# Performance work log

Hardware: AMD Instinct MI355X
Metric: run time of the kernel (lower is better)

## Reference

```python
import jax, jax.numpy as jnp
import numpy as np

MARGIN = 0.25
SCALE = 64.0
OP = 1.0 + MARGIN
ON = -MARGIN
DELTA_P = 1.0 - MARGIN
DELTA_N = MARGIN
NEG_FILL = -1e4  # effectively -inf for these logits (|logit| < ~300)

B, D = 8192, 1024
N_IDS = 512


def setup_inputs() -> dict:
    key = jax.random.key(0)
    k1, k2 = jax.random.split(key)
    inputs = jax.random.normal(k1, (B, D), dtype=jnp.float32)
    targets = jax.random.randint(k2, (B,), 0, N_IDS, dtype=jnp.int64)
    return {"inputs": inputs, "targets": targets}


def reference(inputs, targets):
    # L2-normalize embeddings (torch F.normalize uses eps=1e-12 clamp on norm)
    norm = jnp.maximum(jnp.linalg.norm(inputs, axis=1, keepdims=True), 1e-12)
    x = inputs / norm
    sim = x @ x.T  # [B, B] cosine similarities

    same = targets[:, None] == targets[None, :]
    eye = jnp.eye(targets.shape[0], dtype=bool)
    pos_mask = same & ~eye
    neg_mask = ~same

    sim_sg = jax.lax.stop_gradient(sim)  # .detach() in original
    ap = jnp.maximum(OP - sim_sg, 0.0)
    an = jnp.maximum(sim_sg - ON, 0.0)

    logit_p = -ap * (sim - DELTA_P) * SCALE
    logit_n = an * (sim - DELTA_N) * SCALE

    lse_p = jax.nn.logsumexp(jnp.where(pos_mask, logit_p, NEG_FILL), axis=1)
    lse_n = jax.nn.logsumexp(jnp.where(neg_mask, logit_n, NEG_FILL), axis=1)

    loss_i = jax.nn.softplus(lse_n + lse_p)  # [B]
    valid = pos_mask.any(axis=1) & neg_mask.any(axis=1)

    total = jnp.sum(jnp.where(valid, loss_i, 0.0))
    count = jnp.maximum(jnp.sum(valid), 1)
    return total / count
```

## Files before the change

### kernel.cpp

```cpp
#include <hip/hip_runtime.h>
#include <hip/hip_bf16.h>
#include <math.h>

#define THREADS 256
typedef unsigned short ushortT;
typedef __attribute__((ext_vector_type(8))) short bf16x8;
typedef __attribute__((ext_vector_type(4))) float f32x4;

__device__ __forceinline__ void async16(const ushortT* g, ushortT* l) {
  __builtin_amdgcn_global_load_lds(
      (const __attribute__((address_space(1))) unsigned int*)g,
      (__attribute__((address_space(3))) unsigned int*)l, 16, 0, 0);
}

__device__ __forceinline__ ushortT f2bf(float f) {
  __hip_bfloat16 h = __float2bfloat16(f);
  return *reinterpret_cast<ushortT*>(&h);
}

__global__ __launch_bounds__(THREADS) void k_prep(const float* __restrict__ x,
                                                  ushortT* __restrict__ xn, int D) {
  __shared__ float red[4];
  const int row = blockIdx.x;
  const int tid = threadIdx.x;
  const int gid = row * (D / 4) + tid;
  const float4 v = reinterpret_cast<const float4*>(x)[gid];
  float s = v.x * v.x + v.y * v.y + v.z * v.z + v.w * v.w;
  #pragma unroll
  for (int off = 32; off; off >>= 1) s += __shfl_xor(s, off);
  if ((tid & 63) == 0) red[tid >> 6] = s;
  __syncthreads();
  const float tot = red[0] + red[1] + red[2] + red[3];
  const float rn = 1.0f / fmaxf(sqrtf(tot), 1e-12f);
  ushort4 o;
  o.x = f2bf(v.x * rn); o.y = f2bf(v.y * rn);
  o.z = f2bf(v.z * rn); o.w = f2bf(v.w * rn);
  reinterpret_cast<ushort4*>(xn)[gid] = o;
}

__global__ __launch_bounds__(THREADS, 4) void k_main_mfma(const ushortT* __restrict__ xn,
                                                          const int* __restrict__ tgt,
                                                          float4* __restrict__ partial,
                                                          int D, int nb) {
  __shared__ ushortT Asm[2][128 * 32];
  __shared__ ushortT Bsm[2][128 * 32];

  const int tid = threadIdx.x;
  const int lane = tid & 63;
  const int w = tid >> 6;

  const int b = blockIdx.x;
  int bi = (int)((2.f * nb + 1.f -
                  sqrtf((2.f * nb + 1.f) * (2.f * nb + 1.f) - 8.f * (float)b)) * 0.5f);
  while ((bi + 1) * (2 * nb - bi) / 2 <= b) ++bi;
  while (bi * (2 * nb - bi + 1) / 2 > b) --bi;
  const int bj = bi + (b - bi * (2 * nb - bi + 1) / 2);
  const bool isdiag = (bi == bj);

  const int i0 = bi * 128, j0 = bj * 128;
  const int wr = (w >> 1) * 64, wc = (w & 1) * 64;

  const int sr = lane & 15, sc = lane >> 4;
  const ushortT* gA0 = xn + (size_t)(i0 + w * 16 + sr) * D + sc * 8;
  const ushortT* gA1 = gA0 + (size_t)64 * D;
  const ushortT* gB0 = xn + (size_t)(j0 + w * 16 + sr) * D + sc * 8;
  const ushortT* gB1 = gB0 + (size_t)64 * D;
  const int lo0 = w * 512;
  const int lo1 = (w + 4) * 512;

  const int aoff = ((w >> 1) * 4) * 512 + lane * 8;
  const int boff = ((w & 1) * 4) * 512 + lane * 8;

  f32x4 acc[4][4];
  #pragma unroll
  for (int mt = 0; mt < 4; ++mt)
    #pragma unroll
    for (int nt = 0; nt < 4; ++nt)
      acc[mt][nt] = (f32x4){0.f, 0.f, 0.f, 0.f};

  async16(gA0, &Asm[0][lo0]);
  async16(gA1, &Asm[0][lo1]);
  if (!isdiag) {
    async16(gB0, &Bsm[0][lo0]);
    async16(gB1, &Bsm[0][lo1]);
  }
  __syncthreads();

  const int kiters = D / 32;
  for (int kk = 0; kk < kiters; ++kk) {
    const int cur = kk & 1;
    if (kk + 1 < kiters) {
      const size_t ko = (size_t)(kk + 1) * 32;
      async16(gA0 + ko, &Asm[cur ^ 1][lo0]);
      async16(gA1 + ko, &Asm[cur ^ 1][lo1]);
      if (!isdiag) {
        async16(gB0 + ko, &Bsm[cur ^ 1][lo0]);
        async16(gB1 + ko, &Bsm[cur ^ 1][lo1]);
      }
    }
    const ushortT* Ab = &Asm[cur][0];
    const ushortT* Bb = isdiag ? &Asm[cur][0] : &Bsm[cur][0];
    bf16x8 afr[4], bfr[4];
    #pragma unroll
    for (int mt = 0; mt < 4; ++mt)
      afr[mt] = *reinterpret_cast<const bf16x8*>(&Ab[aoff + mt * 512]);
    #pragma unroll
    for (int nt = 0; nt < 4; ++nt)
      bfr[nt] = *reinterpret_cast<const bf16x8*>(&Bb[boff + nt * 512]);
    #pragma unroll
    for (int mt = 0; mt < 4; ++mt)
      #pragma unroll
      for (int nt = 0; nt < 4; ++nt)
        acc[mt][nt] = __builtin_amdgcn_mfma_f32_16x16x32_bf16(afr[mt], bfr[nt], acc[mt][nt], 0, 0, 0);
    __syncthreads();
  }

  const int q = lane >> 4, c = lane & 15;
  int tj[4];
  #pragma unroll
  for (int nt = 0; nt < 4; ++nt) tj[nt] = tgt[j0 + wc + nt * 16 + c];
  int tir[16];
  #pragma unroll
  for (int mt = 0; mt < 4; ++mt) {
    const int4 t4 = *reinterpret_cast<const int4*>(tgt + i0 + wr + mt * 16 + q * 4);
    tir[mt * 4 + 0] = t4.x; tir[mt * 4 + 1] = t4.y;
    tir[mt * 4 + 2] = t4.z; tir[mt * 4 + 3] = t4.w;
  }

  #pragma unroll
  for (int mt = 0; mt < 4; ++mt) {
    #pragma unroll
    for (int reg = 0; reg < 4; ++reg) {
      const int i = i0 + wr + mt * 16 + q * 4 + reg;
      const int ti = tir[mt * 4 + reg];
      float m = -1e30f, sn = 0.f;
      float sel[4];
      #pragma unroll
      for (int nt = 0; nt < 4; ++nt) {
        const float s = acc[mt][nt][reg];
        const int j = j0 + wc + nt * 16 + c;
        const bool same = (tj[nt] == ti);
        const bool vpos = same && (j != i);
        const float lp = (fminf(s, 1.25f) - 1.25f) * fmaf(s, 64.f, -48.f);
        const float sv = vpos ? lp : -2e30f;
        sel[nt] = sv;
        m = fmaxf(m, sv);
        const float ln = (fmaxf(s, -0.25f) + 0.25f) * fmaf(s, 64.f, -16.f);
        const float en = __expf(ln);
        sn += same ? 0.f : en;
      }
      #pragma unroll
      for (int off = 1; off < 16; off <<= 1) m = fmaxf(m, __shfl_xor(m, off));
      float sp = 0.f;
      #pragma unroll
      for (int nt = 0; nt < 4; ++nt) sp += __expf(sel[nt] - m);
      #pragma unroll
      for (int off = 1; off < 16; off <<= 1) {
        sp += __shfl_xor(sp, off);
        sn += __shfl_xor(sn, off);
      }
      if (c == 0) {
        float4 o; o.x = m; o.y = sp; o.z = 0.f; o.w = sn;
        partial[((size_t)i * nb + bj) * 2 + (w & 1)] = o;
      }
    }
  }

  if (!isdiag) {
    #pragma unroll
    for (int nt = 0; nt < 4; ++nt) {
      const int jt = tj[nt];
      const int jrow = j0 + wc + nt * 16 + c;
      float m = -1e30f, sn = 0.f;
      float sel[16];
      #pragma unroll
      for (int mt = 0; mt < 4; ++mt) {
        #pragma unroll
        for (int reg = 0; reg < 4; ++reg) {
          const float s = acc[mt][nt][reg];
          const bool same = (tir[mt * 4 + reg] == jt);
          const float lp = (fminf(s, 1.25f) - 1.25f) * fmaf(s, 64.f, -48.f);
          const float sv = same ? lp : -2e30f;
          sel[mt * 4 + reg] = sv;
          m = fmaxf(m, sv);
          const float ln = (fmaxf(s, -0.25f) + 0.25f) * fmaf(s, 64.f, -16.f);
          const float en = __expf(ln);
          sn += same ? 0.f : en;
        }
      }
      m = fmaxf(m, __shfl_xor(m, 16));
      m = fmaxf(m, __shfl_xor(m, 32));
      float sp = 0.f;
      #pragma unroll
      for (int k = 0; k < 16; ++k) sp += __expf(sel[k] - m);
      sp += __shfl_xor(sp, 16); sp += __shfl_xor(sp, 32);
      sn += __shfl_xor(sn, 16); sn += __shfl_xor(sn, 32);
      if (lane < 16) {
        float4 o; o.x = m; o.y = sp; o.z = 0.f; o.w = sn;
        partial[((size_t)jrow * nb + bi) * 2 + (w >> 1)] = o;
      }
    }
  }
}

__global__ __launch_bounds__(THREADS) void k_reduce(const float4* __restrict__ partial,
                                                    float* __restrict__ row_loss) {
  const int lane = threadIdx.x & 63;
  const int row = blockIdx.x * 4 + (threadIdx.x >> 6);
  const float4 a = partial[(size_t)row * 128 + lane];
  const float4 b = partial[(size_t)row * 128 + 64 + lane];
  float mp = fmaxf(a.x, b.x);
  float sp = a.y * __expf(a.x - mp) + b.y * __expf(b.x - mp);
  float sn = a.w + b.w;
  #pragma unroll
  for (int off = 1; off < 64; off <<= 1) {
    const float m2 = __shfl_xor(mp, off), s2 = __shfl_xor(sp, off);
    const float nm = fmaxf(mp, m2);
    sp = sp * __expf(mp - nm) + s2 * __expf(m2 - nm);
    mp = nm;
    sn += __shfl_xor(sn, off);
  }
  if (lane == 0) {
    float loss = -1.0f;
    if (sp > 0.f && sn > 0.f) {
      const float z = mp + logf(sp) + logf(sn);
      loss = (z > 0.f) ? (z + log1pf(__expf(-z))) : log1pf(__expf(z));
    }
    row_loss[row] = loss;
  }
}

__global__ __launch_bounds__(THREADS) void k_final(const float* __restrict__ row_loss,
                                                   float* __restrict__ out, int B) {
  __shared__ float ssum[4];
  __shared__ float scnt[4];
  const int tid = threadIdx.x;
  float sum = 0.f, cnt = 0.f;
  for (int i = tid; i < B; i += THREADS) {
    const float l = row_loss[i];
    if (l >= 0.f) { sum += l; cnt += 1.f; }
  }
  #pragma unroll
  for (int off = 32; off; off >>= 1) {
    sum += __shfl_xor(sum, off);
    cnt += __shfl_xor(cnt, off);
  }
  if ((tid & 63) == 0) { ssum[tid >> 6] = sum; scnt[tid >> 6] = cnt; }
  __syncthreads();
  if (tid == 0) {
    float ts = 0.f, tc = 0.f;
    #pragma unroll
    for (int w = 0; w < 4; ++w) { ts += ssum[w]; tc += scnt[w]; }
    out[0] = ts / fmaxf(tc, 1.f);
  }
}

extern "C" void kernel_launch(void* const* d_in, const int* in_sizes, int n_in,
                              void* d_out, int out_size, void* d_ws, size_t ws_size,
                              hipStream_t stream) {
  const float* x = (const float*)d_in[0];
  const int* tgt = (const int*)d_in[1];
  float* out = (float*)d_out;
  const int B = in_sizes[1];
  const int D = in_sizes[0] / B;
  const int nb = B / 128;

  ushortT* xn = (ushortT*)d_ws;
  float4* partial = (float4*)((char*)d_ws + (size_t)B * D * 2);
  float* row_loss = (float*)((char*)d_ws + (size_t)B * D * 2 + (size_t)B * 2 * nb * 16);

  k_prep<<<B, THREADS, 0, stream>>>(x, xn, D);
  k_main_mfma<<<nb * (nb + 1) / 2, THREADS, 0, stream>>>(xn, tgt, partial, D, nb);
  k_reduce<<<B / 4, THREADS, 0, stream>>>(partial, row_loss);
  k_final<<<1, THREADS, 0, stream>>>(row_loss, out, B);
}
```

Before: 259.6 us.

## Swizzle triangular tile order and merge half-tile partials in LDS before store

Replaces the closed-form triangular block mapping with a super-tile (8x8 groups) ordering so that concurrently running blocks share row/column strips in cache. The two per-wave-column partial (max, sum) records are combined in shared memory, reusing the A tile buffer, and one float4 per row per tile is written in a column-major [nb][B] layout. This halves the partial-buffer writes and lets the reduce kernel read one record per lane. The cost is an extra __syncthreads, more index arithmetic per block, and a mapping that hardcodes nb=64 (36 super-tiles of 8).

```diff
diff --git a/kernel.cpp b/kernel.cpp
--- a/kernel.cpp
+++ b/kernel.cpp
@@ -41,7 +41,7 @@
 __global__ __launch_bounds__(THREADS, 4) void k_main_mfma(const ushortT* __restrict__ xn,
                                                           const int* __restrict__ tgt,
                                                           float4* __restrict__ partial,
-                                                          int D, int nb) {
+                                                          int D, int B) {
   __shared__ ushortT Asm[2][128 * 32];
   __shared__ ushortT Bsm[2][128 * 32];
 
@@ -50,11 +50,28 @@
   const int w = tid >> 6;
 
   const int b = blockIdx.x;
-  int bi = (int)((2.f * nb + 1.f -
-                  sqrtf((2.f * nb + 1.f) * (2.f * nb + 1.f) - 8.f * (float)b)) * 0.5f);
-  while ((bi + 1) * (2 * nb - bi) / 2 <= b) ++bi;
-  while (bi * (2 * nb - bi + 1) / 2 > b) --bi;
-  const int bj = bi + (b - bi * (2 * nb - bi + 1) / 2);
+  int base = 0, SI = 0, SJ = 0, found = 0;
+  for (int x = 0; x < 8 && !found; ++x) {
+    for (int ss = x; ss < 36; ss += 8) {
+      int si = 0, rem = ss;
+      while (rem >= 8 - si) { rem -= 8 - si; ++si; }
+      const int sj = si + rem;
+      const int size = (si == sj) ? 36 : 64;
+      if (b < base + size) { SI = si; SJ = sj; found = 1; break; }
+      base += size;
+    }
+  }
+  const int l = b - base;
+  int li, lj;
+  if (SI == SJ) {
+    int t = l, row = 0;
+    while (t >= 8 - row) { t -= 8 - row; ++row; }
+    li = row; lj = row + t;
+  } else {
+    li = l >> 3; lj = l & 7;
+  }
+  const int bi = SI * 8 + li;
+  const int bj = SJ * 8 + lj;
   const bool isdiag = (bi == bj);
 
   const int i0 = bi * 128, j0 = bj * 128;
@@ -127,11 +144,15 @@
     tir[mt * 4 + 2] = t4.z; tir[mt * 4 + 3] = t4.w;
   }
 
+  float4* eo1 = reinterpret_cast<float4*>(&Asm[0][0]);
+  float4* eo2 = reinterpret_cast<float4*>(&Asm[0][2048]);
+
   #pragma unroll
   for (int mt = 0; mt < 4; ++mt) {
     #pragma unroll
     for (int reg = 0; reg < 4; ++reg) {
-      const int i = i0 + wr + mt * 16 + q * 4 + reg;
+      const int il = wr + mt * 16 + q * 4 + reg;
+      const int i = i0 + il;
       const int ti = tir[mt * 4 + reg];
       float m = -1e30f, sn = 0.f;
       float sel[4];
@@ -160,8 +181,8 @@
         sn += __shfl_xor(sn, off);
       }
       if (c == 0) {
-        float4 o; o.x = m; o.y = sp; o.z = 0.f; o.w = sn;
-        partial[((size_t)i * nb + bj) * 2 + (w & 1)] = o;
+        float4 o; o.x = m; o.y = sp; o.z = sn; o.w = 0.f;
+        eo1[il * 2 + (w & 1)] = o;
       }
     }
   }
@@ -170,7 +191,6 @@
     #pragma unroll
     for (int nt = 0; nt < 4; ++nt) {
       const int jt = tj[nt];
-      const int jrow = j0 + wc + nt * 16 + c;
       float m = -1e30f, sn = 0.f;
       float sel[16];
       #pragma unroll
@@ -196,22 +216,43 @@
       sp += __shfl_xor(sp, 16); sp += __shfl_xor(sp, 32);
       sn += __shfl_xor(sn, 16); sn += __shfl_xor(sn, 32);
       if (lane < 16) {
-        float4 o; o.x = m; o.y = sp; o.z = 0.f; o.w = sn;
-        partial[((size_t)jrow * nb + bi) * 2 + (w >> 1)] = o;
-      }
-    }
+        float4 o; o.x = m; o.y = sp; o.z = sn; o.w = 0.f;
+        eo2[(wc + nt * 16 + lane) * 2 + (w >> 1)] = o;
+      }
+    }
+  }
+
+  __syncthreads();
+
+  if (tid < 128) {
+    const float4 a = eo1[tid * 2], bb = eo1[tid * 2 + 1];
+    const float m = fmaxf(a.x, bb.x);
+    float4 o;
+    o.x = m;
+    o.y = a.y * __expf(a.x - m) + bb.y * __expf(bb.x - m);
+    o.z = a.z + bb.z;
+    o.w = 0.f;
+    partial[(size_t)bj * B + i0 + tid] = o;
+  } else if (!isdiag) {
+    const int t = tid - 128;
+    const float4 a = eo2[t * 2], bb = eo2[t * 2 + 1];
+    const float m = fmaxf(a.x, bb.x);
+    float4 o;
+    o.x = m;
+    o.y = a.y * __expf(a.x - m) + bb.y * __expf(bb.x - m);
+    o.z = a.z + bb.z;
+    o.w = 0.f;
+    partial[(size_t)bi * B + j0 + t] = o;
   }
 }
 
 __global__ __launch_bounds__(THREADS) void k_reduce(const float4* __restrict__ partial,
-                                                    float* __restrict__ row_loss) {
+                                                    float* __restrict__ row_loss,
+                                                    int B) {
   const int lane = threadIdx.x & 63;
   const int row = blockIdx.x * 4 + (threadIdx.x >> 6);
-  const float4 a = partial[(size_t)row * 128 + lane];
-  const float4 b = partial[(size_t)row * 128 + 64 + lane];
-  float mp = fmaxf(a.x, b.x);
-  float sp = a.y * __expf(a.x - mp) + b.y * __expf(b.x - mp);
-  float sn = a.w + b.w;
+  const float4 p = partial[(size_t)lane * B + row];
+  float mp = p.x, sp = p.y, sn = p.z;
   #pragma unroll
   for (int off = 1; off < 64; off <<= 1) {
     const float m2 = __shfl_xor(mp, off), s2 = __shfl_xor(sp, off);
@@ -267,10 +308,10 @@
 
   ushortT* xn = (ushortT*)d_ws;
   float4* partial = (float4*)((char*)d_ws + (size_t)B * D * 2);
-  float* row_loss = (float*)((char*)d_ws + (size_t)B * D * 2 + (size_t)B * 2 * nb * 16);
+  float* row_loss = (float*)((char*)d_ws + (size_t)B * D * 2 + (size_t)nb * B * 16);
 
   k_prep<<<B, THREADS, 0, stream>>>(x, xn, D);
-  k_main_mfma<<<nb * (nb + 1) / 2, THREADS, 0, stream>>>(xn, tgt, partial, D, nb);
-  k_reduce<<<B / 4, THREADS, 0, stream>>>(partial, row_loss);
+  k_main_mfma<<<nb * (nb + 1) / 2, THREADS, 0, stream>>>(xn, tgt, partial, D, B);
+  k_reduce<<<B / 4, THREADS, 0, stream>>>(partial, row_loss, B);
   k_final<<<1, THREADS, 0, stream>>>(row_loss, out, B);
 }
```

Measured after the change: 261.9 us. No clear change (+0.9%).

## Use 256x128 tiles with per-wave 64x128 MFMA subtiles and transposed partials

Applied to the files above, without the earlier changes.

Each block now computes a 256-row by 128-column tile of the upper-triangular similarity matrix. Each wave owns 64 rows across all 128 columns, so B fragments are shared across more MFMAs and each block issues fewer loads per output. Column-side partials are combined across waves in shared memory before being written, and the partial buffer is laid out column-block-major so k_reduce reads one entry per lane. The per-row logits are recomputed in a second pass instead of being held in a sel array. The cost is a larger accumulator, 128 floats per thread, with occupancy lowered to 2 waves per SIMD. Diagonal-straddling tiles also recompute some redundant lower-triangle work.

```diff
diff --git a/kernel.cpp b/kernel.cpp
--- a/kernel.cpp
+++ b/kernel.cpp
@@ -38,91 +38,98 @@
   reinterpret_cast<ushort4*>(xn)[gid] = o;
 }
 
-__global__ __launch_bounds__(THREADS, 4) void k_main_mfma(const ushortT* __restrict__ xn,
+__global__ __launch_bounds__(THREADS, 2) void k_main_mfma(const ushortT* __restrict__ xn,
                                                           const int* __restrict__ tgt,
                                                           float4* __restrict__ partial,
-                                                          int D, int nb) {
-  __shared__ ushortT Asm[2][128 * 32];
-  __shared__ ushortT Bsm[2][128 * 32];
+                                                          int D, int B) {
+  __shared__ ushortT Asm[2][16 * 512];
+  __shared__ ushortT Bsm[2][8 * 512];
 
   const int tid = threadIdx.x;
   const int lane = tid & 63;
   const int w = tid >> 6;
 
+  const int NRB = B / 256;
+  const int C1 = 2 * NRB + 1;
   const int b = blockIdx.x;
-  int bi = (int)((2.f * nb + 1.f -
-                  sqrtf((2.f * nb + 1.f) * (2.f * nb + 1.f) - 8.f * (float)b)) * 0.5f);
-  while ((bi + 1) * (2 * nb - bi) / 2 <= b) ++bi;
-  while (bi * (2 * nb - bi + 1) / 2 > b) --bi;
-  const int bj = bi + (b - bi * (2 * nb - bi + 1) / 2);
-  const bool isdiag = (bi == bj);
-
-  const int i0 = bi * 128, j0 = bj * 128;
-  const int wr = (w >> 1) * 64, wc = (w & 1) * 64;
+  int rb = (int)((C1 - sqrtf((float)(C1 * C1 - 4 * b))) * 0.5f);
+  while (rb * (C1 - rb) > b) --rb;
+  while ((rb + 1) * (C1 - rb - 1) <= b) ++rb;
+  const int cb = 2 * rb + (b - rb * (C1 - rb));
+  const bool ndiag = (cb <= 2 * rb + 1);
+
+  const int i0 = rb * 256, j0 = cb * 128;
 
   const int sr = lane & 15, sc = lane >> 4;
-  const ushortT* gA0 = xn + (size_t)(i0 + w * 16 + sr) * D + sc * 8;
-  const ushortT* gA1 = gA0 + (size_t)64 * D;
-  const ushortT* gB0 = xn + (size_t)(j0 + w * 16 + sr) * D + sc * 8;
-  const ushortT* gB1 = gB0 + (size_t)64 * D;
-  const int lo0 = w * 512;
-  const int lo1 = (w + 4) * 512;
-
-  const int aoff = ((w >> 1) * 4) * 512 + lane * 8;
-  const int boff = ((w & 1) * 4) * 512 + lane * 8;
-
-  f32x4 acc[4][4];
+  const ushortT* gA[4];
+  #pragma unroll
+  for (int t = 0; t < 4; ++t)
+    gA[t] = xn + (size_t)(i0 + 16 * (4 * w + t) + sr) * D + sc * 8;
+  const ushortT* gB[2];
+  #pragma unroll
+  for (int u = 0; u < 2; ++u)
+    gB[u] = xn + (size_t)(j0 + 16 * (w + 4 * u) + sr) * D + sc * 8;
+
+  f32x4 acc[4][8];
   #pragma unroll
   for (int mt = 0; mt < 4; ++mt)
     #pragma unroll
-    for (int nt = 0; nt < 4; ++nt)
+    for (int nt = 0; nt < 8; ++nt)
       acc[mt][nt] = (f32x4){0.f, 0.f, 0.f, 0.f};
 
-  async16(gA0, &Asm[0][lo0]);
-  async16(gA1, &Asm[0][lo1]);
-  if (!isdiag) {
-    async16(gB0, &Bsm[0][lo0]);
-    async16(gB1, &Bsm[0][lo1]);
+  #pragma unroll
+  for (int t = 0; t < 4; ++t) async16(gA[t], &Asm[0][(4 * w + t) * 512]);
+  if (!ndiag) {
+    #pragma unroll
+    for (int u = 0; u < 2; ++u) async16(gB[u], &Bsm[0][(w + 4 * u) * 512]);
   }
   __syncthreads();
 
+  const int boffg = ndiag ? (cb - 2 * rb) * 8 : 0;
   const int kiters = D / 32;
   for (int kk = 0; kk < kiters; ++kk) {
     const int cur = kk & 1;
     if (kk + 1 < kiters) {
       const size_t ko = (size_t)(kk + 1) * 32;
-      async16(gA0 + ko, &Asm[cur ^ 1][lo0]);
-      async16(gA1 + ko, &Asm[cur ^ 1][lo1]);
-      if (!isdiag) {
-        async16(gB0 + ko, &Bsm[cur ^ 1][lo0]);
-        async16(gB1 + ko, &Bsm[cur ^ 1][lo1]);
+      #pragma unroll
+      for (int t = 0; t < 4; ++t)
+        async16(gA[t] + ko, &Asm[cur ^ 1][(4 * w + t) * 512]);
+      if (!ndiag) {
+        #pragma unroll
+        for (int u = 0; u < 2; ++u)
+          async16(gB[u] + ko, &Bsm[cur ^ 1][(w + 4 * u) * 512]);
       }
     }
     const ushortT* Ab = &Asm[cur][0];
-    const ushortT* Bb = isdiag ? &Asm[cur][0] : &Bsm[cur][0];
-    bf16x8 afr[4], bfr[4];
+    const ushortT* Bb = ndiag ? &Asm[cur][boffg * 512] : &Bsm[cur][0];
+    bf16x8 afr[4];
     #pragma unroll
     for (int mt = 0; mt < 4; ++mt)
-      afr[mt] = *reinterpret_cast<const bf16x8*>(&Ab[aoff + mt * 512]);
-    #pragma unroll
-    for (int nt = 0; nt < 4; ++nt)
-      bfr[nt] = *reinterpret_cast<const bf16x8*>(&Bb[boff + nt * 512]);
-    #pragma unroll
-    for (int mt = 0; mt < 4; ++mt)
-      #pragma unroll
-      for (int nt = 0; nt < 4; ++nt)
-        acc[mt][nt] = __builtin_amdgcn_mfma_f32_16x16x32_bf16(afr[mt], bfr[nt], acc[mt][nt], 0, 0, 0);
+      afr[mt] = *reinterpret_cast<const bf16x8*>(&Ab[(4 * w + mt) * 512 + lane * 8]);
+    #pragma unroll
+    for (int h = 0; h < 2; ++h) {
+      bf16x8 bfr[4];
+      #pragma unroll
+      for (int n4 = 0; n4 < 4; ++n4)
+        bfr[n4] = *reinterpret_cast<const bf16x8*>(&Bb[(h * 4 + n4) * 512 + lane * 8]);
+      #pragma unroll
+      for (int mt = 0; mt < 4; ++mt)
+        #pragma unroll
+        for (int n4 = 0; n4 < 4; ++n4)
+          acc[mt][h * 4 + n4] =
+              __builtin_amdgcn_mfma_f32_16x16x32_bf16(afr[mt], bfr[n4], acc[mt][h * 4 + n4], 0, 0, 0);
+    }
     __syncthreads();
   }
 
   const int q = lane >> 4, c = lane & 15;
-  int tj[4];
-  #pragma unroll
-  for (int nt = 0; nt < 4; ++nt) tj[nt] = tgt[j0 + wc + nt * 16 + c];
+  int tj[8];
+  #pragma unroll
+  for (int nt = 0; nt < 8; ++nt) tj[nt] = tgt[j0 + nt * 16 + c];
   int tir[16];
   #pragma unroll
   for (int mt = 0; mt < 4; ++mt) {
-    const int4 t4 = *reinterpret_cast<const int4*>(tgt + i0 + wr + mt * 16 + q * 4);
+    const int4 t4 = *reinterpret_cast<const int4*>(tgt + i0 + w * 64 + mt * 16 + q * 4);
     tir[mt * 4 + 0] = t4.x; tir[mt * 4 + 1] = t4.y;
     tir[mt * 4 + 2] = t4.z; tir[mt * 4 + 3] = t4.w;
   }
@@ -131,87 +138,105 @@
   for (int mt = 0; mt < 4; ++mt) {
     #pragma unroll
     for (int reg = 0; reg < 4; ++reg) {
-      const int i = i0 + wr + mt * 16 + q * 4 + reg;
+      const int i = i0 + w * 64 + mt * 16 + q * 4 + reg;
       const int ti = tir[mt * 4 + reg];
       float m = -1e30f, sn = 0.f;
-      float sel[4];
-      #pragma unroll
-      for (int nt = 0; nt < 4; ++nt) {
+      #pragma unroll
+      for (int nt = 0; nt < 8; ++nt) {
         const float s = acc[mt][nt][reg];
-        const int j = j0 + wc + nt * 16 + c;
+        const int j = j0 + nt * 16 + c;
         const bool same = (tj[nt] == ti);
-        const bool vpos = same && (j != i);
+        const bool v = same && (j != i);
         const float lp = (fminf(s, 1.25f) - 1.25f) * fmaf(s, 64.f, -48.f);
-        const float sv = vpos ? lp : -2e30f;
-        sel[nt] = sv;
-        m = fmaxf(m, sv);
+        m = v ? fmaxf(m, lp) : m;
         const float ln = (fmaxf(s, -0.25f) + 0.25f) * fmaf(s, 64.f, -16.f);
-        const float en = __expf(ln);
-        sn += same ? 0.f : en;
+        sn += same ? 0.f : __expf(ln);
       }
       #pragma unroll
       for (int off = 1; off < 16; off <<= 1) m = fmaxf(m, __shfl_xor(m, off));
       float sp = 0.f;
       #pragma unroll
-      for (int nt = 0; nt < 4; ++nt) sp += __expf(sel[nt] - m);
+      for (int nt = 0; nt < 8; ++nt) {
+        const float s = acc[mt][nt][reg];
+        const int j = j0 + nt * 16 + c;
+        const bool v = (tj[nt] == ti) && (j != i);
+        const float lp = (fminf(s, 1.25f) - 1.25f) * fmaf(s, 64.f, -48.f);
+        sp += v ? __expf(lp - m) : 0.f;
+      }
       #pragma unroll
       for (int off = 1; off < 16; off <<= 1) {
         sp += __shfl_xor(sp, off);
         sn += __shfl_xor(sn, off);
       }
       if (c == 0) {
-        float4 o; o.x = m; o.y = sp; o.z = 0.f; o.w = sn;
-        partial[((size_t)i * nb + bj) * 2 + (w & 1)] = o;
-      }
-    }
-  }
-
-  if (!isdiag) {
-    #pragma unroll
-    for (int nt = 0; nt < 4; ++nt) {
+        float4 o; o.x = m; o.y = sp; o.z = sn; o.w = 0.f;
+        partial[(size_t)cb * B + i] = o;
+      }
+    }
+  }
+
+  if (!ndiag) {
+    float4* eo = reinterpret_cast<float4*>(&Asm[0][0]);
+    #pragma unroll
+    for (int nt = 0; nt < 8; ++nt) {
       const int jt = tj[nt];
-      const int jrow = j0 + wc + nt * 16 + c;
       float m = -1e30f, sn = 0.f;
-      float sel[16];
-      #pragma unroll
-      for (int mt = 0; mt < 4; ++mt) {
+      #pragma unroll
+      for (int mt = 0; mt < 4; ++mt)
         #pragma unroll
         for (int reg = 0; reg < 4; ++reg) {
           const float s = acc[mt][nt][reg];
           const bool same = (tir[mt * 4 + reg] == jt);
           const float lp = (fminf(s, 1.25f) - 1.25f) * fmaf(s, 64.f, -48.f);
-          const float sv = same ? lp : -2e30f;
-          sel[mt * 4 + reg] = sv;
-          m = fmaxf(m, sv);
+          m = same ? fmaxf(m, lp) : m;
           const float ln = (fmaxf(s, -0.25f) + 0.25f) * fmaf(s, 64.f, -16.f);
-          const float en = __expf(ln);
-          sn += same ? 0.f : en;
+          sn += same ? 0.f : __expf(ln);
         }
-      }
       m = fmaxf(m, __shfl_xor(m, 16));
       m = fmaxf(m, __shfl_xor(m, 32));
       float sp = 0.f;
       #pragma unroll
-      for (int k = 0; k < 16; ++k) sp += __expf(sel[k] - m);
+      for (int mt = 0; mt < 4; ++mt)
+        #pragma unroll
+        for (int reg = 0; reg < 4; ++reg) {
+          const float s = acc[mt][nt][reg];
+          const bool same = (tir[mt * 4 + reg] == jt);
+          const float lp = (fminf(s, 1.25f) - 1.25f) * fmaf(s, 64.f, -48.f);
+          sp += same ? __expf(lp - m) : 0.f;
+        }
       sp += __shfl_xor(sp, 16); sp += __shfl_xor(sp, 32);
       sn += __shfl_xor(sn, 16); sn += __shfl_xor(sn, 32);
-      if (lane < 16) {
-        float4 o; o.x = m; o.y = sp; o.z = 0.f; o.w = sn;
-        partial[((size_t)jrow * nb + bi) * 2 + (w >> 1)] = o;
-      }
+      if (q == 0) {
+        float4 o; o.x = m; o.y = sp; o.z = sn; o.w = 0.f;
+        eo[w * 128 + nt * 16 + c] = o;
+      }
+    }
+    __syncthreads();
+    if (tid < 128) {
+      float mm = -1e30f, ms = 0.f, mn = 0.f;
+      #pragma unroll
+      for (int ww = 0; ww < 4; ++ww) {
+        const float4 p = eo[ww * 128 + tid];
+        const float nm = fmaxf(mm, p.x);
+        ms = ms * __expf(mm - nm) + p.y * __expf(p.x - nm);
+        mm = nm;
+        mn += p.z;
+      }
+      float4 o; o.x = mm; o.y = ms; o.z = mn; o.w = 0.f;
+      partial[(size_t)(2 * rb) * B + j0 + tid] = o;
+      float4 z; z.x = -1e30f; z.y = 0.f; z.z = 0.f; z.w = 0.f;
+      partial[(size_t)(2 * rb + 1) * B + j0 + tid] = z;
     }
   }
 }
 
 __global__ __launch_bounds__(THREADS) void k_reduce(const float4* __restrict__ partial,
-                                                    float* __restrict__ row_loss) {
+                                                    float* __restrict__ row_loss,
+                                                    int B) {
   const int lane = threadIdx.x & 63;
   const int row = blockIdx.x * 4 + (threadIdx.x >> 6);
-  const float4 a = partial[(size_t)row * 128 + lane];
-  const float4 b = partial[(size_t)row * 128 + 64 + lane];
-  float mp = fmaxf(a.x, b.x);
-  float sp = a.y * __expf(a.x - mp) + b.y * __expf(b.x - mp);
-  float sn = a.w + b.w;
+  const float4 p = partial[(size_t)lane * B + row];
+  float mp = p.x, sp = p.y, sn = p.z;
   #pragma unroll
   for (int off = 1; off < 64; off <<= 1) {
     const float m2 = __shfl_xor(mp, off), s2 = __shfl_xor(sp, off);
@@ -263,14 +288,15 @@
   float* out = (float*)d_out;
   const int B = in_sizes[1];
   const int D = in_sizes[0] / B;
-  const int nb = B / 128;
+  const int NRB = B / 256;
+  const int nblocks = NRB * (2 * NRB + 1) - NRB * NRB;
 
   ushortT* xn = (ushortT*)d_ws;
   float4* partial = (float4*)((char*)d_ws + (size_t)B * D * 2);
-  float* row_loss = (float*)((char*)d_ws + (size_t)B * D * 2 + (size_t)B * 2 * nb * 16);
+  float* row_loss = (float*)((char*)d_ws + (size_t)B * D * 2 + (size_t)(B / 128) * B * 16);
 
   k_prep<<<B, THREADS, 0, stream>>>(x, xn, D);
-  k_main_mfma<<<nb * (nb + 1) / 2, THREADS, 0, stream>>>(xn, tgt, partial, D, nb);
-  k_reduce<<<B / 4, THREADS, 0, stream>>>(partial, row_loss);
+  k_main_mfma<<<nblocks, THREADS, 0, stream>>>(xn, tgt, partial, D, B);
+  k_reduce<<<B / 4, THREADS, 0, stream>>>(partial, row_loss, B);
   k_final<<<1, THREADS, 0, stream>>>(row_loss, out, B);
 }
```

Result: slower. 279.2 us (+7.5%).
